# Kernel optimization log

Hardware: AMD Instinct MI355X
Metric: run time of the kernel (lower is better)

Reference implementation:

```python
import jax, jax.numpy as jnp
import numpy as np

NEG_SLOPE = 0.2

def _gatv2_layer(x, src, tgt, Wl, Wr, att, bias, num_nodes, heads, ch):
    # x: [N, Fin]; src/tgt: [E] (self loops already included)
    xl = (x @ Wl).reshape(num_nodes, heads, ch)  # source transform [N,H,C]
    xr = (x @ Wr).reshape(num_nodes, heads, ch)  # target transform [N,H,C]
    m = xl[src] + xr[tgt]                        # [E,H,C]
    m = jnp.where(m > 0, m, NEG_SLOPE * m)       # LeakyReLU
    e = jnp.einsum('ehc,hc->eh', m, att)         # attention logits [E,H]
    # softmax over incoming edges of each target node (numerically stable)
    e_max = jax.ops.segment_max(e, tgt, num_segments=num_nodes)
    e_max = jnp.where(jnp.isfinite(e_max), e_max, 0.0)
    alpha = jnp.exp(e - e_max[tgt])              # [E,H]
    denom = jax.ops.segment_sum(alpha, tgt, num_segments=num_nodes)
    alpha = alpha / (denom[tgt] + 1e-16)
    out = jax.ops.segment_sum(alpha[:, :, None] * xl[src], tgt, num_segments=num_nodes)  # [N,H,C]
    return out.mean(axis=1) + bias               # concat=False -> mean over heads, then bias


def setup_inputs() -> dict:
    key = jax.random.key(0)
    ks = jax.random.split(key, 12)
    N, E = 50000, 800000
    IN, HID, H = 128, 64, 2
    features = jax.random.normal(ks[0], (N, IN), dtype=jnp.float32)
    edge_index = jax.random.randint(ks[1], (2, E), 0, N, dtype=jnp.int64)
    s = 0.1
    return {
        'features': features,
        'edge_index': edge_index,
        'Wl1': jax.random.normal(ks[2], (IN, H * HID), dtype=jnp.float32) * s,
        'Wr1': jax.random.normal(ks[3], (IN, H * HID), dtype=jnp.float32) * s,
        'att1': jax.random.normal(ks[4], (H, HID), dtype=jnp.float32) * s,
        'b1': jnp.zeros((HID,), dtype=jnp.float32),
        'Wl2': jax.random.normal(ks[5], (HID, H * HID), dtype=jnp.float32) * s,
        'Wr2': jax.random.normal(ks[6], (HID, H * HID), dtype=jnp.float32) * s,
        'att2': jax.random.normal(ks[7], (H, HID), dtype=jnp.float32) * s,
        'b2': jnp.zeros((HID,), dtype=jnp.float32),
    }


def reference(features, edge_index, Wl1, Wr1, att1, b1, Wl2, Wr2, att2, b2):
    N = features.shape[0]
    H, HID = att1.shape
    # PyG GATv2Conv default add_self_loops=True
    loop = jnp.arange(N, dtype=edge_index.dtype)
    src = jnp.concatenate([edge_index[0], loop])
    tgt = jnp.concatenate([edge_index[1], loop])
    h = _gatv2_layer(features, src, tgt, Wl1, Wr1, att1, b1, N, H, HID)
    h = jax.nn.relu(h)
    out = _gatv2_layer(h, src, tgt, Wl2, Wr2, att2, b2, N, H, HID)
    return out  # node_mask in original is None
```

## Files before the change

kernel.cpp:

```cpp
#include <hip/hip_runtime.h>
#include <hip/hip_bf16.h>
#include <math.h>


#define HEADS 2
#define CH 64
#define FDIM (HEADS * CH)
#define CAP 48
#define HBLK 3328

typedef _Float16 f16_t;
typedef _Float16 f16x4 __attribute__((ext_vector_type(4)));
typedef _Float16 f16x8 __attribute__((ext_vector_type(8)));
typedef float f32x4 __attribute__((ext_vector_type(4)));


__global__ __launch_bounds__(256)
void init_kernel(const float* __restrict__ Wl1, const float* __restrict__ Wr1,
                 const float* __restrict__ Wl2, const float* __restrict__ Wr2,
                 f16_t* __restrict__ fl1, f16_t* __restrict__ fr1,
                 f16_t* __restrict__ fl2, f16_t* __restrict__ fr2,
                 int* __restrict__ cnt, int N) {
    int bx = blockIdx.x;
    if (bx < 4) {
        const float* W; f16_t* F; int K;
        switch (bx) {
            case 0:  W = Wl1; F = fl1; K = 128; break;
            case 1:  W = Wr1; F = fr1; K = 128; break;
            case 2:  W = Wl2; F = fl2; K = 64;  break;
            default: W = Wr2; F = fr2; K = 64;  break;
        }
        int S = K >> 5;
        int total = 8 * S * 64;
        for (int idx = threadIdx.x; idx < total; idx += blockDim.x) {
            int l  = idx & 63;
            int ts = idx >> 6;
            int s  = ts % S;
            int t  = ts / S;
            int n  = t * 16 + (l & 15);
            int k0 = s * 32 + (l >> 4) * 8;
            f16x8 v;
            #pragma unroll
            for (int j = 0; j < 8; ++j) v[j] = (f16_t)W[(size_t)(k0 + j) * 128 + n];
            *(f16x8*)(F + (size_t)idx * 8) = v;
        }
    } else {
        int n4 = (N + 3) >> 2;
        int stride = (gridDim.x - 4) * blockDim.x;
        for (int i = (bx - 4) * blockDim.x + threadIdx.x; i < n4; i += stride) {
            int i0 = i * 4;
            if (i0 + 3 < N) *(int4*)(cnt + i0) = make_int4(0, 0, 0, 0);
            else for (int k = 0; k < 4 && i0 + k < N; ++k) cnt[i0 + k] = 0;
        }
    }
}


__device__ __forceinline__ unsigned int pack_bf16x2(float x, float y) {
    __hip_bfloat16 lo = __float2bfloat16(x);
    __hip_bfloat16 hi = __float2bfloat16(y);
    unsigned short ulo = *reinterpret_cast<unsigned short*>(&lo);
    unsigned short uhi = *reinterpret_cast<unsigned short*>(&hi);
    return ((unsigned int)uhi << 16) | ulo;
}

__device__ __forceinline__
void gemm_body(const float* __restrict__ X,
               const f16_t* __restrict__ FL, const f16_t* __restrict__ FR,
               unsigned int* __restrict__ Y0b, float* __restrict__ Y1,
               int N, int K, int gblk, float* lds_f) {
    f16_t* Af = (f16_t*)lds_f;
    int tid  = threadIdx.x;
    int lane = tid & 63;
    int wave = tid >> 6;
    int row0 = gblk * 32;
    int S = K >> 5;

    {
        int r  = tid >> 3;
        int m  = r & 15;
        int g  = r >> 4;
        int gr = row0 + r;
        int kc = (tid & 7) * (K >> 3);
        const float* xp = X + (size_t)gr * K + kc;
        f16_t* areg = Af + g * (16 * K);
        for (int c = 0; c < (K >> 3); c += 4) {
            float4 xv = make_float4(0.f, 0.f, 0.f, 0.f);
            if (gr < N) xv = *(const float4*)(xp + c);
            int k = kc + c;
            int s = k >> 5;
            int lanei = ((k >> 3) & 3) * 16 + m;
            int j = k & 7;
            f16x4 h;
            h[0] = (f16_t)xv.x; h[1] = (f16_t)xv.y;
            h[2] = (f16_t)xv.z; h[3] = (f16_t)xv.w;
            *(f16x4*)(areg + ((s * 64 + lanei) * 8 + j)) = h;
        }
    }
    __syncthreads();

    int rg  = wave >> 1;
    int mat = wave & 1;
    const f16_t* F = mat ? FR : FL;

    f32x4 acc[8];
    #pragma unroll
    for (int t = 0; t < 8; ++t) acc[t] = (f32x4){0.f, 0.f, 0.f, 0.f};

    const f16_t* aw = Af + rg * (16 * K);
    for (int s = 0; s < S; ++s) {
        f16x8 a = *(const f16x8*)(aw + (s * 64 + lane) * 8);
        #pragma unroll
        for (int t = 0; t < 8; ++t) {
            f16x8 b = *(const f16x8*)(F + ((size_t)(t * S + s) * 64 + lane) * 8);
            acc[t] = __builtin_amdgcn_mfma_f32_16x16x32_f16(a, b, acc[t], 0, 0, 0);
        }
    }
    __syncthreads();

    float* ew = lds_f + wave * (16 * 68);
    int mrow = (lane >> 4) * 4;
    int ccol = lane & 15;
    int rr = lane & 15;
    int ch = lane >> 4;
    int gr2 = row0 + rg * 16 + rr;

    #pragma unroll
    for (int h = 0; h < 2; ++h) {
        #pragma unroll
        for (int tt = 0; tt < 4; ++tt)
            #pragma unroll
            for (int r = 0; r < 4; ++r)
                ew[(mrow + r) * 68 + tt * 16 + ccol] = acc[h * 4 + tt][r];
        __syncthreads();
        if (gr2 < N) {
            const float* src = ew + rr * 68 + ch * 16;
            if (mat == 0) {
                uint4 o0, o1;
                o0.x = pack_bf16x2(src[0],  src[1]);
                o0.y = pack_bf16x2(src[2],  src[3]);
                o0.z = pack_bf16x2(src[4],  src[5]);
                o0.w = pack_bf16x2(src[6],  src[7]);
                o1.x = pack_bf16x2(src[8],  src[9]);
                o1.y = pack_bf16x2(src[10], src[11]);
                o1.z = pack_bf16x2(src[12], src[13]);
                o1.w = pack_bf16x2(src[14], src[15]);
                unsigned int* dst = Y0b + (size_t)gr2 * (FDIM / 2) + h * 32 + ch * 8;
                *(uint4*)dst       = o0;
                *(uint4*)(dst + 4) = o1;
            } else {
                float* dst = Y1 + (size_t)gr2 * FDIM + h * 64 + ch * 16;
                #pragma unroll
                for (int q = 0; q < 4; ++q)
                    *(float4*)(dst + q * 4) = *(const float4*)(src + q * 4);
            }
        }
        __syncthreads();
    }
}

__global__ __launch_bounds__(256)
void fused_scatter_gemm_kernel(const float* __restrict__ X,
                               const f16_t* __restrict__ FL,
                               const f16_t* __restrict__ FR,
                               unsigned int* __restrict__ Y0b,
                               float* __restrict__ Y1,
                               int N, int K,
                               const int* __restrict__ ei, int* __restrict__ cnt,
                               int* __restrict__ ssrc, int E) {
    __shared__ float lds_f[4352];

    if (blockIdx.x < HBLK) {
        int vb   = blockIdx.x;
        int part = vb & 7;
        int blk  = vb >> 3;
        int nblk = HBLK >> 3;
        int lo = (int)(((long long)N * part) >> 3);
        int hi = (int)(((long long)N * (part + 1)) >> 3);
        int stride = nblk * blockDim.x;
        int G = E >> 2;
        for (int g = blk * blockDim.x + threadIdx.x; g < G; g += stride) {
            int4 t4 = *(const int4*)(ei + E + g * 4);
            if (t4.x >= lo && t4.x < hi) {
                int k = atomicAdd(&cnt[t4.x], 1);
                if (k < CAP) ssrc[t4.x * CAP + k] = ei[g * 4 + 0];
            }
            if (t4.y >= lo && t4.y < hi) {
                int k = atomicAdd(&cnt[t4.y], 1);
                if (k < CAP) ssrc[t4.y * CAP + k] = ei[g * 4 + 1];
            }
            if (t4.z >= lo && t4.z < hi) {
                int k = atomicAdd(&cnt[t4.z], 1);
                if (k < CAP) ssrc[t4.z * CAP + k] = ei[g * 4 + 2];
            }
            if (t4.w >= lo && t4.w < hi) {
                int k = atomicAdd(&cnt[t4.w], 1);
                if (k < CAP) ssrc[t4.w * CAP + k] = ei[g * 4 + 3];
            }
        }
        for (int e = (G << 2) + blk * blockDim.x + threadIdx.x; e < E; e += stride) {
            int t = ei[E + e];
            if (t >= lo && t < hi) {
                int k = atomicAdd(&cnt[t], 1);
                if (k < CAP) ssrc[t * CAP + k] = ei[e];
            }
        }
        for (int n = lo + blk * blockDim.x + threadIdx.x; n < hi; n += stride) {
            int k = atomicAdd(&cnt[n], 1);
            if (k < CAP) ssrc[n * CAP + k] = n;
        }
        return;
    }

    gemm_body(X, FL, FR, Y0b, Y1, N, K, blockIdx.x - HBLK, lds_f);
}

__global__ __launch_bounds__(256)
void gemm_kernel(const float* __restrict__ X,
                 const f16_t* __restrict__ FL, const f16_t* __restrict__ FR,
                 unsigned int* __restrict__ Y0b, float* __restrict__ Y1,
                 int N, int K) {
    __shared__ float lds_f[4352];
    gemm_body(X, FL, FR, Y0b, Y1, N, K, blockIdx.x, lds_f);
}


__device__ __forceinline__ void unpack_bf16x2(unsigned int u, float& x, float& y) {
    x = __uint_as_float(u << 16);
    y = __uint_as_float(u & 0xFFFF0000u);
}

__device__ __forceinline__ float2 lrelu2(float2 t) {
    t.x = fmaxf(t.x, 0.2f * t.x);
    t.y = fmaxf(t.y, 0.2f * t.y);
    return t;
}

__global__ __launch_bounds__(256)
void agg_kernel(const unsigned int* __restrict__ xlb, const float* __restrict__ xr,
                const int* __restrict__ cnt, const int* __restrict__ ssrc,
                const float* __restrict__ att, const float* __restrict__ bias,
                float* __restrict__ out, int N, int do_relu) {
    int node = blockIdx.x * 4 + (threadIdx.x >> 6);
    int lane = threadIdx.x & 63;
    if (node >= N) return;

    float2 xr2 = *(const float2*)(xr + (size_t)node * FDIM + 2 * lane);
    float2 a2  = *(const float2*)(att + 2 * lane);

    int beg = node * CAP;
    int deg = cnt[node];
    deg = min(deg, CAP);
    int end = beg + deg;

    float l = 0.f;
    float2 acc = make_float2(0.f, 0.f);

    bool b0 = (lane & 1) != 0;
    bool b1 = (lane & 2) != 0;
    bool b2 = (lane & 4) != 0;
    int base = lane & 32;

    int i = beg;
    int n8 = beg + (deg & ~7);
    for (; i < n8; i += 8) {
        int s0 = min(max(ssrc[i + 0], 0), N - 1);
        int s1 = min(max(ssrc[i + 1], 0), N - 1);
        int s2 = min(max(ssrc[i + 2], 0), N - 1);
        int s3 = min(max(ssrc[i + 3], 0), N - 1);
        int s4 = min(max(ssrc[i + 4], 0), N - 1);
        int s5 = min(max(ssrc[i + 5], 0), N - 1);
        int s6 = min(max(ssrc[i + 6], 0), N - 1);
        int s7 = min(max(ssrc[i + 7], 0), N - 1);
        unsigned int u0 = xlb[(size_t)s0 * (FDIM / 2) + lane];
        unsigned int u1 = xlb[(size_t)s1 * (FDIM / 2) + lane];
        unsigned int u2 = xlb[(size_t)s2 * (FDIM / 2) + lane];
        unsigned int u3 = xlb[(size_t)s3 * (FDIM / 2) + lane];
        unsigned int u4 = xlb[(size_t)s4 * (FDIM / 2) + lane];
        unsigned int u5 = xlb[(size_t)s5 * (FDIM / 2) + lane];
        unsigned int u6 = xlb[(size_t)s6 * (FDIM / 2) + lane];
        unsigned int u7 = xlb[(size_t)s7 * (FDIM / 2) + lane];
        float2 v0, v1, v2, v3, v4, v5, v6, v7;
        unpack_bf16x2(u0, v0.x, v0.y);
        unpack_bf16x2(u1, v1.x, v1.y);
        unpack_bf16x2(u2, v2.x, v2.y);
        unpack_bf16x2(u3, v3.x, v3.y);
        unpack_bf16x2(u4, v4.x, v4.y);
        unpack_bf16x2(u5, v5.x, v5.y);
        unpack_bf16x2(u6, v6.x, v6.y);
        unpack_bf16x2(u7, v7.x, v7.y);

        float2 t0 = lrelu2(make_float2(v0.x + xr2.x, v0.y + xr2.y));
        float2 t1 = lrelu2(make_float2(v1.x + xr2.x, v1.y + xr2.y));
        float2 t2 = lrelu2(make_float2(v2.x + xr2.x, v2.y + xr2.y));
        float2 t3 = lrelu2(make_float2(v3.x + xr2.x, v3.y + xr2.y));
        float2 t4 = lrelu2(make_float2(v4.x + xr2.x, v4.y + xr2.y));
        float2 t5 = lrelu2(make_float2(v5.x + xr2.x, v5.y + xr2.y));
        float2 t6 = lrelu2(make_float2(v6.x + xr2.x, v6.y + xr2.y));
        float2 t7 = lrelu2(make_float2(v7.x + xr2.x, v7.y + xr2.y));
        float p0 = fmaf(t0.x, a2.x, t0.y * a2.y);
        float p1 = fmaf(t1.x, a2.x, t1.y * a2.y);
        float p2 = fmaf(t2.x, a2.x, t2.y * a2.y);
        float p3 = fmaf(t3.x, a2.x, t3.y * a2.y);
        float p4 = fmaf(t4.x, a2.x, t4.y * a2.y);
        float p5 = fmaf(t5.x, a2.x, t5.y * a2.y);
        float p6 = fmaf(t6.x, a2.x, t6.y * a2.y);
        float p7 = fmaf(t7.x, a2.x, t7.y * a2.y);

        float s01 = (b0 ? p1 : p0) + __shfl_xor(b0 ? p0 : p1, 1, 64);
        float s23 = (b0 ? p3 : p2) + __shfl_xor(b0 ? p2 : p3, 1, 64);
        float s45 = (b0 ? p5 : p4) + __shfl_xor(b0 ? p4 : p5, 1, 64);
        float s67 = (b0 ? p7 : p6) + __shfl_xor(b0 ? p6 : p7, 1, 64);
        float q03 = (b1 ? s23 : s01) + __shfl_xor(b1 ? s01 : s23, 2, 64);
        float q47 = (b1 ? s67 : s45) + __shfl_xor(b1 ? s45 : s67, 2, 64);
        float r = (b2 ? q47 : q03) + __shfl_xor(b2 ? q03 : q47, 4, 64);
        r += __shfl_xor(r, 8, 64);
        r += __shfl_xor(r, 16, 64);

        float a = __expf(r);
        float al0 = __shfl(a, base | 0, 64);
        float al1 = __shfl(a, base | 1, 64);
        float al2 = __shfl(a, base | 2, 64);
        float al3 = __shfl(a, base | 3, 64);
        float al4 = __shfl(a, base | 4, 64);
        float al5 = __shfl(a, base | 5, 64);
        float al6 = __shfl(a, base | 6, 64);
        float al7 = __shfl(a, base | 7, 64);

        acc.x = fmaf(al0, v0.x, acc.x); acc.y = fmaf(al0, v0.y, acc.y);
        acc.x = fmaf(al1, v1.x, acc.x); acc.y = fmaf(al1, v1.y, acc.y);
        acc.x = fmaf(al2, v2.x, acc.x); acc.y = fmaf(al2, v2.y, acc.y);
        acc.x = fmaf(al3, v3.x, acc.x); acc.y = fmaf(al3, v3.y, acc.y);
        acc.x = fmaf(al4, v4.x, acc.x); acc.y = fmaf(al4, v4.y, acc.y);
        acc.x = fmaf(al5, v5.x, acc.x); acc.y = fmaf(al5, v5.y, acc.y);
        acc.x = fmaf(al6, v6.x, acc.x); acc.y = fmaf(al6, v6.y, acc.y);
        acc.x = fmaf(al7, v7.x, acc.x); acc.y = fmaf(al7, v7.y, acc.y);
        l += ((al0 + al1) + (al2 + al3)) + ((al4 + al5) + (al6 + al7));
    }
    int n4 = i + ((end - i) & ~3);
    for (; i < n4; i += 4) {
        int s0 = min(max(ssrc[i + 0], 0), N - 1);
        int s1 = min(max(ssrc[i + 1], 0), N - 1);
        int s2 = min(max(ssrc[i + 2], 0), N - 1);
        int s3 = min(max(ssrc[i + 3], 0), N - 1);
        unsigned int u0 = xlb[(size_t)s0 * (FDIM / 2) + lane];
        unsigned int u1 = xlb[(size_t)s1 * (FDIM / 2) + lane];
        unsigned int u2 = xlb[(size_t)s2 * (FDIM / 2) + lane];
        unsigned int u3 = xlb[(size_t)s3 * (FDIM / 2) + lane];
        float2 v0, v1, v2, v3;
        unpack_bf16x2(u0, v0.x, v0.y);
        unpack_bf16x2(u1, v1.x, v1.y);
        unpack_bf16x2(u2, v2.x, v2.y);
        unpack_bf16x2(u3, v3.x, v3.y);

        float2 t0 = lrelu2(make_float2(v0.x + xr2.x, v0.y + xr2.y));
        float2 t1 = lrelu2(make_float2(v1.x + xr2.x, v1.y + xr2.y));
        float2 t2 = lrelu2(make_float2(v2.x + xr2.x, v2.y + xr2.y));
        float2 t3 = lrelu2(make_float2(v3.x + xr2.x, v3.y + xr2.y));
        float p0 = fmaf(t0.x, a2.x, t0.y * a2.y);
        float p1 = fmaf(t1.x, a2.x, t1.y * a2.y);
        float p2 = fmaf(t2.x, a2.x, t2.y * a2.y);
        float p3 = fmaf(t3.x, a2.x, t3.y * a2.y);

        float s01 = (b0 ? p1 : p0) + __shfl_xor(b0 ? p0 : p1, 1, 64);
        float s23 = (b0 ? p3 : p2) + __shfl_xor(b0 ? p2 : p3, 1, 64);
        float q = (b1 ? s23 : s01) + __shfl_xor(b1 ? s01 : s23, 2, 64);
        q += __shfl_xor(q, 4, 64);
        q += __shfl_xor(q, 8, 64);
        q += __shfl_xor(q, 16, 64);
        float a = __expf(q);
        float al0 = __shfl(a, base | 0, 64);
        float al1 = __shfl(a, base | 1, 64);
        float al2 = __shfl(a, base | 2, 64);
        float al3 = __shfl(a, base | 3, 64);

        acc.x = fmaf(al0, v0.x, acc.x); acc.y = fmaf(al0, v0.y, acc.y);
        acc.x = fmaf(al1, v1.x, acc.x); acc.y = fmaf(al1, v1.y, acc.y);
        acc.x = fmaf(al2, v2.x, acc.x); acc.y = fmaf(al2, v2.y, acc.y);
        acc.x = fmaf(al3, v3.x, acc.x); acc.y = fmaf(al3, v3.y, acc.y);
        l += (al0 + al1) + (al2 + al3);
    }
    for (; i < end; ++i) {
        int s = min(max(ssrc[i], 0), N - 1);
        unsigned int u = xlb[(size_t)s * (FDIM / 2) + lane];
        float2 v;
        unpack_bf16x2(u, v.x, v.y);
        float2 t = lrelu2(make_float2(v.x + xr2.x, v.y + xr2.y));
        float p = fmaf(t.x, a2.x, t.y * a2.y);
        #pragma unroll
        for (int d = 1; d < 32; d <<= 1) p += __shfl_xor(p, d, 64);
        float al = __expf(p);
        acc.x = fmaf(al, v.x, acc.x);
        acc.y = fmaf(al, v.y, acc.y);
        l += al;
    }

    float inv = 1.0f / (l + 1e-16f);
    float rx = acc.x * inv;
    float ry = acc.y * inv;
    float ox = 0.5f * (rx + __shfl_xor(rx, 32, 64));
    float oy = 0.5f * (ry + __shfl_xor(ry, 32, 64));
    if (lane < 32) {
        float2 b = *(const float2*)(bias + 2 * lane);
        ox += b.x; oy += b.y;
        if (do_relu) { ox = fmaxf(ox, 0.f); oy = fmaxf(oy, 0.f); }
        *(float2*)(out + (size_t)node * CH + 2 * lane) = make_float2(ox, oy);
    }
}


static inline size_t align_up(size_t x, size_t a) { return (x + a - 1) & ~(a - 1); }

extern "C" void kernel_launch(void* const* d_in, const int* in_sizes, int n_in,
                              void* d_out, int out_size, void* d_ws, size_t ws_size,
                              hipStream_t stream) {
    const float* features = (const float*)d_in[0];
    const int*   ei       = (const int*)d_in[1];
    const float* Wl1      = (const float*)d_in[2];
    const float* Wr1      = (const float*)d_in[3];
    const float* att1     = (const float*)d_in[4];
    const float* b1       = (const float*)d_in[5];
    const float* Wl2      = (const float*)d_in[6];
    const float* Wr2      = (const float*)d_in[7];
    const float* att2     = (const float*)d_in[8];
    const float* b2       = (const float*)d_in[9];

    int N = in_sizes[0] / FDIM;
    int E = in_sizes[1] / 2;

    char* w = (char*)d_ws;
    int* cnt      = (int*)w;  w += align_up((size_t)N * 4, 256);
    int* ssrc     = (int*)w;  w += align_up((size_t)N * CAP * 4, 256);
    unsigned int* xlb = (unsigned int*)w; w += align_up((size_t)N * (FDIM / 2) * 4, 256);
    float* xr     = (float*)w; w += align_up((size_t)N * FDIM * 4, 256);
    float* hbuf   = (float*)w; w += align_up((size_t)N * CH * 4, 256);
    f16_t* fl1    = (f16_t*)w; w += align_up((size_t)8 * 4 * 64 * 8 * 2, 256);
    f16_t* fr1    = (f16_t*)w; w += align_up((size_t)8 * 4 * 64 * 8 * 2, 256);
    f16_t* fl2    = (f16_t*)w; w += align_up((size_t)8 * 2 * 64 * 8 * 2, 256);
    f16_t* fr2    = (f16_t*)w; w += align_up((size_t)8 * 2 * 64 * 8 * 2, 256);

    int gblocks = (N + 31) / 32;
    dim3 agrid((N + 3) / 4);

    init_kernel<<<56, 256, 0, stream>>>(Wl1, Wr1, Wl2, Wr2,
                                        fl1, fr1, fl2, fr2, cnt, N);

    fused_scatter_gemm_kernel<<<HBLK + gblocks, 256, 0, stream>>>(
        features, fl1, fr1, xlb, xr, N, 128, ei, cnt, ssrc, E);
    agg_kernel<<<agrid, 256, 0, stream>>>(xlb, xr, cnt, ssrc, att1, b1, hbuf, N, 1);

    gemm_kernel<<<gblocks, 256, 0, stream>>>(hbuf, fl2, fr2, xlb, xr, N, 64);
    agg_kernel<<<agrid, 256, 0, stream>>>(xlb, xr, cnt, ssrc, att2, b2, (float*)d_out, N, 0);
}
```

Before: 251.0 us.

## Fuse layer-1 aggregation with layer-2 GEMM and drop source index clamps

Adds an agg_gemm_kernel in which each block aggregates 32 nodes for layer 1, keeps the ReLU'd hidden rows in LDS, and then runs the layer-2 MFMA projection on them directly. This removes the hbuf round trip through global memory and one kernel launch, and it uses double-buffered xl/xr outputs when the workspace is large enough. The ssrc clamping is also removed from the aggregation loops, which saves integer ops but trusts the scattered indices to be valid. The cost is that the fused kernel launches only N/32 blocks, each walking 8 nodes per wave in sequence, so it has less parallelism for hiding gather latency than the old 4-nodes-per-block aggregation.

Measured after the change: 275.4 us. +9.7%, slower.

```diff
diff --git a/kernel.cpp b/kernel.cpp
--- a/kernel.cpp
+++ b/kernel.cpp
@@ -236,17 +236,11 @@
     return t;
 }
 
-__global__ __launch_bounds__(256)
-void agg_kernel(const unsigned int* __restrict__ xlb, const float* __restrict__ xr,
+__device__ __forceinline__
+float2 agg_node(const unsigned int* __restrict__ xlb, const float* __restrict__ xr,
                 const int* __restrict__ cnt, const int* __restrict__ ssrc,
-                const float* __restrict__ att, const float* __restrict__ bias,
-                float* __restrict__ out, int N, int do_relu) {
-    int node = blockIdx.x * 4 + (threadIdx.x >> 6);
-    int lane = threadIdx.x & 63;
-    if (node >= N) return;
-
+                float2 a2, int node, int lane) {
     float2 xr2 = *(const float2*)(xr + (size_t)node * FDIM + 2 * lane);
-    float2 a2  = *(const float2*)(att + 2 * lane);
 
     int beg = node * CAP;
     int deg = cnt[node];
@@ -264,14 +258,14 @@
     int i = beg;
     int n8 = beg + (deg & ~7);
     for (; i < n8; i += 8) {
-        int s0 = min(max(ssrc[i + 0], 0), N - 1);
-        int s1 = min(max(ssrc[i + 1], 0), N - 1);
-        int s2 = min(max(ssrc[i + 2], 0), N - 1);
-        int s3 = min(max(ssrc[i + 3], 0), N - 1);
-        int s4 = min(max(ssrc[i + 4], 0), N - 1);
-        int s5 = min(max(ssrc[i + 5], 0), N - 1);
-        int s6 = min(max(ssrc[i + 6], 0), N - 1);
-        int s7 = min(max(ssrc[i + 7], 0), N - 1);
+        int s0 = ssrc[i + 0];
+        int s1 = ssrc[i + 1];
+        int s2 = ssrc[i + 2];
+        int s3 = ssrc[i + 3];
+        int s4 = ssrc[i + 4];
+        int s5 = ssrc[i + 5];
+        int s6 = ssrc[i + 6];
+        int s7 = ssrc[i + 7];
         unsigned int u0 = xlb[(size_t)s0 * (FDIM / 2) + lane];
         unsigned int u1 = xlb[(size_t)s1 * (FDIM / 2) + lane];
         unsigned int u2 = xlb[(size_t)s2 * (FDIM / 2) + lane];
@@ -339,10 +333,10 @@
     }
     int n4 = i + ((end - i) & ~3);
     for (; i < n4; i += 4) {
-        int s0 = min(max(ssrc[i + 0], 0), N - 1);
-        int s1 = min(max(ssrc[i + 1], 0), N - 1);
-        int s2 = min(max(ssrc[i + 2], 0), N - 1);
-        int s3 = min(max(ssrc[i + 3], 0), N - 1);
+        int s0 = ssrc[i + 0];
+        int s1 = ssrc[i + 1];
+        int s2 = ssrc[i + 2];
+        int s3 = ssrc[i + 3];
         unsigned int u0 = xlb[(size_t)s0 * (FDIM / 2) + lane];
         unsigned int u1 = xlb[(size_t)s1 * (FDIM / 2) + lane];
         unsigned int u2 = xlb[(size_t)s2 * (FDIM / 2) + lane];
@@ -381,7 +375,7 @@
         l += (al0 + al1) + (al2 + al3);
     }
     for (; i < end; ++i) {
-        int s = min(max(ssrc[i], 0), N - 1);
+        int s = ssrc[i];
         unsigned int u = xlb[(size_t)s * (FDIM / 2) + lane];
         float2 v;
         unpack_bf16x2(u, v.x, v.y);
@@ -396,15 +390,148 @@
     }
 
     float inv = 1.0f / (l + 1e-16f);
-    float rx = acc.x * inv;
-    float ry = acc.y * inv;
-    float ox = 0.5f * (rx + __shfl_xor(rx, 32, 64));
-    float oy = 0.5f * (ry + __shfl_xor(ry, 32, 64));
+    return make_float2(acc.x * inv, acc.y * inv);
+}
+
+__global__ __launch_bounds__(256)
+void agg_kernel(const unsigned int* __restrict__ xlb, const float* __restrict__ xr,
+                const int* __restrict__ cnt, const int* __restrict__ ssrc,
+                const float* __restrict__ att, const float* __restrict__ bias,
+                float* __restrict__ out, int N, int do_relu) {
+    int node = blockIdx.x * 4 + (threadIdx.x >> 6);
+    int lane = threadIdx.x & 63;
+    if (node >= N) return;
+
+    float2 a2 = *(const float2*)(att + 2 * lane);
+    float2 r = agg_node(xlb, xr, cnt, ssrc, a2, node, lane);
+    float ox = 0.5f * (r.x + __shfl_xor(r.x, 32, 64));
+    float oy = 0.5f * (r.y + __shfl_xor(r.y, 32, 64));
     if (lane < 32) {
         float2 b = *(const float2*)(bias + 2 * lane);
         ox += b.x; oy += b.y;
         if (do_relu) { ox = fmaxf(ox, 0.f); oy = fmaxf(oy, 0.f); }
         *(float2*)(out + (size_t)node * CH + 2 * lane) = make_float2(ox, oy);
+    }
+}
+
+
+__global__ __launch_bounds__(256)
+void agg_gemm_kernel(const unsigned int* __restrict__ xlb, const float* __restrict__ xr,
+                     const int* __restrict__ cnt, const int* __restrict__ ssrc,
+                     const float* __restrict__ att, const float* __restrict__ bias,
+                     const f16_t* __restrict__ FL, const f16_t* __restrict__ FR,
+                     unsigned int* __restrict__ Y0b, float* __restrict__ Y1, int N) {
+    __shared__ float lds_f[4352];
+    __shared__ float hrows[32 * 68];
+    const int K = 64;
+    const int S = 2;
+
+    int tid  = threadIdx.x;
+    int lane = tid & 63;
+    int wave = tid >> 6;
+    int row0 = blockIdx.x * 32;
+
+    float2 a2 = *(const float2*)(att + 2 * lane);
+    float2 bv = make_float2(0.f, 0.f);
+    if (lane < 32) bv = *(const float2*)(bias + 2 * lane);
+
+    for (int q = 0; q < 8; ++q) {
+        int ln   = wave * 8 + q;
+        int node = row0 + ln;
+        float ox = 0.f, oy = 0.f;
+        if (node < N) {
+            float2 r = agg_node(xlb, xr, cnt, ssrc, a2, node, lane);
+            ox = 0.5f * (r.x + __shfl_xor(r.x, 32, 64));
+            oy = 0.5f * (r.y + __shfl_xor(r.y, 32, 64));
+            ox = fmaxf(ox + bv.x, 0.f);
+            oy = fmaxf(oy + bv.y, 0.f);
+        }
+        if (lane < 32)
+            *(float2*)(hrows + ln * 68 + 2 * lane) = make_float2(ox, oy);
+    }
+    __syncthreads();
+
+    f16_t* Af = (f16_t*)lds_f;
+    {
+        int r  = tid >> 3;
+        int m  = r & 15;
+        int g  = r >> 4;
+        int kc = (tid & 7) * 8;
+        const float* xp = hrows + r * 68 + kc;
+        f16_t* areg = Af + g * (16 * K);
+        #pragma unroll
+        for (int c = 0; c < 8; c += 4) {
+            float4 xv = *(const float4*)(xp + c);
+            int k = kc + c;
+            int s = k >> 5;
+            int lanei = ((k >> 3) & 3) * 16 + m;
+            int j = k & 7;
+            f16x4 h;
+            h[0] = (f16_t)xv.x; h[1] = (f16_t)xv.y;
+            h[2] = (f16_t)xv.z; h[3] = (f16_t)xv.w;
+            *(f16x4*)(areg + ((s * 64 + lanei) * 8 + j)) = h;
+        }
+    }
+    __syncthreads();
+
+    int rg  = wave >> 1;
+    int mat = wave & 1;
+    const f16_t* F = mat ? FR : FL;
+
+    f32x4 acc[8];
+    #pragma unroll
+    for (int t = 0; t < 8; ++t) acc[t] = (f32x4){0.f, 0.f, 0.f, 0.f};
+
+    const f16_t* aw = Af + rg * (16 * K);
+    #pragma unroll
+    for (int s = 0; s < S; ++s) {
+        f16x8 a = *(const f16x8*)(aw + (s * 64 + lane) * 8);
+        #pragma unroll
+        for (int t = 0; t < 8; ++t) {
+            f16x8 b = *(const f16x8*)(F + ((size_t)(t * S + s) * 64 + lane) * 8);
+            acc[t] = __builtin_amdgcn_mfma_f32_16x16x32_f16(a, b, acc[t], 0, 0, 0);
+        }
+    }
+    __syncthreads();
+
+    float* ew = lds_f + wave * (16 * 68);
+    int mrow = (lane >> 4) * 4;
+    int ccol = lane & 15;
+    int rr = lane & 15;
+    int ch = lane >> 4;
+    int gr2 = row0 + rg * 16 + rr;
+
+    #pragma unroll
+    for (int h = 0; h < 2; ++h) {
+        #pragma unroll
+        for (int tt = 0; tt < 4; ++tt)
+            #pragma unroll
+            for (int r = 0; r < 4; ++r)
+                ew[(mrow + r) * 68 + tt * 16 + ccol] = acc[h * 4 + tt][r];
+        __syncthreads();
+        if (gr2 < N) {
+            const float* src = ew + rr * 68 + ch * 16;
+            if (mat == 0) {
+                uint4 o0, o1;
+                o0.x = pack_bf16x2(src[0],  src[1]);
+                o0.y = pack_bf16x2(src[2],  src[3]);
+                o0.z = pack_bf16x2(src[4],  src[5]);
+                o0.w = pack_bf16x2(src[6],  src[7]);
+                o1.x = pack_bf16x2(src[8],  src[9]);
+                o1.y = pack_bf16x2(src[10], src[11]);
+                o1.z = pack_bf16x2(src[12], src[13]);
+                o1.w = pack_bf16x2(src[14], src[15]);
+                unsigned int* dst = Y0b + (size_t)gr2 * (FDIM / 2) + h * 32 + ch * 8;
+                *(uint4*)dst       = o0;
+                *(uint4*)(dst + 4) = o1;
+            } else {
+                float* dst = Y1 + (size_t)gr2 * FDIM + h * 64 + ch * 16;
+                #pragma unroll
+                for (int q = 0; q < 4; ++q)
+                    *(float4*)(dst + q * 4) = *(const float4*)(src + q * 4);
+            }
+        }
+        __syncthreads();
     }
 }
 
@@ -428,27 +555,55 @@
     int N = in_sizes[0] / FDIM;
     int E = in_sizes[1] / 2;
 
+    size_t sz_cnt  = align_up((size_t)N * 4, 256);
+    size_t sz_ssrc = align_up((size_t)N * CAP * 4, 256);
+    size_t sz_xlb  = align_up((size_t)N * (FDIM / 2) * 4, 256);
+    size_t sz_xr   = align_up((size_t)N * FDIM * 4, 256);
+    size_t sz_h    = align_up((size_t)N * CH * 4, 256);
+    size_t sz_f128 = align_up((size_t)8 * 4 * 64 * 8 * 2, 256);
+    size_t sz_f64  = align_up((size_t)8 * 2 * 64 * 8 * 2, 256);
+
     char* w = (char*)d_ws;
-    int* cnt      = (int*)w;  w += align_up((size_t)N * 4, 256);
-    int* ssrc     = (int*)w;  w += align_up((size_t)N * CAP * 4, 256);
-    unsigned int* xlb = (unsigned int*)w; w += align_up((size_t)N * (FDIM / 2) * 4, 256);
-    float* xr     = (float*)w; w += align_up((size_t)N * FDIM * 4, 256);
-    float* hbuf   = (float*)w; w += align_up((size_t)N * CH * 4, 256);
-    f16_t* fl1    = (f16_t*)w; w += align_up((size_t)8 * 4 * 64 * 8 * 2, 256);
-    f16_t* fr1    = (f16_t*)w; w += align_up((size_t)8 * 4 * 64 * 8 * 2, 256);
-    f16_t* fl2    = (f16_t*)w; w += align_up((size_t)8 * 2 * 64 * 8 * 2, 256);
-    f16_t* fr2    = (f16_t*)w; w += align_up((size_t)8 * 2 * 64 * 8 * 2, 256);
+    int* cnt          = (int*)w;          w += sz_cnt;
+    int* ssrc         = (int*)w;          w += sz_ssrc;
+    unsigned int* xlb = (unsigned int*)w; w += sz_xlb;
+    float* xr         = (float*)w;        w += sz_xr;
+
+    size_t need_fused = sz_cnt + sz_ssrc + 2 * sz_xlb + 2 * sz_xr
+                      + 2 * sz_f128 + 2 * sz_f64;
 
     int gblocks = (N + 31) / 32;
     dim3 agrid((N + 3) / 4);
 
-    init_kernel<<<56, 256, 0, stream>>>(Wl1, Wr1, Wl2, Wr2,
-                                        fl1, fr1, fl2, fr2, cnt, N);
-
-    fused_scatter_gemm_kernel<<<HBLK + gblocks, 256, 0, stream>>>(
-        features, fl1, fr1, xlb, xr, N, 128, ei, cnt, ssrc, E);
-    agg_kernel<<<agrid, 256, 0, stream>>>(xlb, xr, cnt, ssrc, att1, b1, hbuf, N, 1);
-
-    gemm_kernel<<<gblocks, 256, 0, stream>>>(hbuf, fl2, fr2, xlb, xr, N, 64);
-    agg_kernel<<<agrid, 256, 0, stream>>>(xlb, xr, cnt, ssrc, att2, b2, (float*)d_out, N, 0);
-}
+    if (ws_size >= need_fused) {
+        unsigned int* xlb2 = (unsigned int*)w; w += sz_xlb;
+        float* xr2         = (float*)w;        w += sz_xr;
+        f16_t* fl1 = (f16_t*)w; w += sz_f128;
+        f16_t* fr1 = (f16_t*)w; w += sz_f128;
+        f16_t* fl2 = (f16_t*)w; w += sz_f64;
+        f16_t* fr2 = (f16_t*)w; w += sz_f64;
+
+        init_kernel<<<56, 256, 0, stream>>>(Wl1, Wr1, Wl2, Wr2,
+                                            fl1, fr1, fl2, fr2, cnt, N);
+        fused_scatter_gemm_kernel<<<HBLK + gblocks, 256, 0, stream>>>(
+            features, fl1, fr1, xlb, xr, N, 128, ei, cnt, ssrc, E);
+        agg_gemm_kernel<<<gblocks, 256, 0, stream>>>(
+            xlb, xr, cnt, ssrc, att1, b1, fl2, fr2, xlb2, xr2, N);
+        agg_kernel<<<agrid, 256, 0, stream>>>(
+            xlb2, xr2, cnt, ssrc, att2, b2, (float*)d_out, N, 0);
+    } else {
+        float* hbuf = (float*)w; w += sz_h;
+        f16_t* fl1 = (f16_t*)w; w += sz_f128;
+        f16_t* fr1 = (f16_t*)w; w += sz_f128;
+        f16_t* fl2 = (f16_t*)w; w += sz_f64;
+        f16_t* fr2 = (f16_t*)w; w += sz_f64;
+
+        init_kernel<<<56, 256, 0, stream>>>(Wl1, Wr1, Wl2, Wr2,
+                                            fl1, fr1, fl2, fr2, cnt, N);
+        fused_scatter_gemm_kernel<<<HBLK + gblocks, 256, 0, stream>>>(
+            features, fl1, fr1, xlb, xr, N, 128, ei, cnt, ssrc, E);
+        agg_kernel<<<agrid, 256, 0, stream>>>(xlb, xr, cnt, ssrc, att1, b1, hbuf, N, 1);
+        gemm_kernel<<<gblocks, 256, 0, stream>>>(hbuf, fl2, fr2, xlb, xr, N, 64);
+        agg_kernel<<<agrid, 256, 0, stream>>>(xlb, xr, cnt, ssrc, att2, b2, (float*)d_out, N, 0);
+    }
+}
```
